# Kernel tuning notes

Hardware: AMD Instinct MI355X
Metric: run time of the kernel (lower is better)

Reference implementation:

```python
import jax, jax.numpy as jnp
import numpy as np

B, T, L, DC, DW, H, V = 128, 256, 4, 128, 128, 256, 6000
NEG = -1e30

def _lstm(x, c, h, kernel, bias):
    # TF BasicLSTMCell, forget_bias=0, gate order i, j, f, o
    z = jnp.concatenate([x, h], axis=-1) @ kernel + bias
    i, j, f, o = jnp.split(z, 4, axis=-1)
    nc = c * jax.nn.sigmoid(f) + jax.nn.sigmoid(i) * jnp.tanh(j)
    nh = jnp.tanh(nc) * jax.nn.sigmoid(o)
    return nc, nh

def _forward(chars, char_emb, reset_W, reset_b, com_W, com_b, lstm_kernel, lstm_bias, pred_W, pred_b, score_U, bos):
    Bn, Tn = chars.shape
    dt = char_emb.dtype
    # init agenda entry: BoS vector through LSTM from zero state
    c0 = jnp.zeros((Bn, H), dt)
    h0 = jnp.zeros((Bn, H), dt)
    x0 = jnp.broadcast_to(bos, (Bn, DW))
    c1, h1 = _lstm(x0, c0, h0, lstm_kernel, lstm_bias)
    pred0 = jnp.tanh(h1 @ pred_W + pred_b)
    # rolling buffer over the last L agenda entries (slot w-1 = position t-w)
    buf_pred = jnp.repeat(pred0[:, None, :], L, axis=1)
    buf_c = jnp.repeat(c1[:, None, :], L, axis=1)
    buf_h = jnp.repeat(h1[:, None, :], L, axis=1)
    # windows[t, b, j] = char at position t-j (age j), front-padded
    padded = jnp.pad(chars, ((0, 0), (L - 1, 0)))
    gi = jnp.arange(Tn)[:, None] + (L - 1) - jnp.arange(L)[None, :]
    windows = jnp.transpose(padded[:, gi], (1, 0, 2))  # [T, B, L]
    wlens = jnp.arange(1, L + 1)
    cmask = (jnp.arange(L)[None, :] < wlens[:, None]).astype(dt)  # [W, C]
    inv_len = (1.0 / wlens).astype(dt)

    def step(carry, xs):
        buf_pred, buf_c, buf_h = carry
        window, t = xs
        emb = char_emb[window]  # [B, L, DC] (ages 0..L-1)
        # per-wlen reset gate (separate weights per word length)
        g = jax.nn.sigmoid(jnp.einsum('bcd,wde->bwce', emb, reset_W) + reset_b[None, :, None, :])
        proj = jnp.tanh(jnp.einsum('bwcd,de->bwce', g * emb[:, None], com_W) + com_b)  # [B,W,C,DW]
        word = jnp.einsum('bwce,wc->bwe', proj, cmask) * inv_len[None, :, None]  # [B,W,DW] mean over the wlen chars
        score = jnp.sum((buf_pred + score_U) * word, axis=-1)  # [B,W] local score vs prev prediction
        score = jnp.where((wlens <= t + 1)[None, :], score, NEG)
        best = jnp.argmax(score, axis=1)  # greedy choice of word length
        b3 = best[:, None, None]
        word_b = jnp.take_along_axis(word, b3, axis=1)[:, 0]
        c_prev = jnp.take_along_axis(buf_c, b3, axis=1)[:, 0]
        h_prev = jnp.take_along_axis(buf_h, b3, axis=1)[:, 0]
        nc, nh = _lstm(word_b, c_prev, h_prev, lstm_kernel, lstm_bias)
        npred = jnp.tanh(nh @ pred_W + pred_b)
        carry = (jnp.concatenate([npred[:, None], buf_pred[:, :-1]], axis=1),
                 jnp.concatenate([nc[:, None], buf_c[:, :-1]], axis=1),
                 jnp.concatenate([nh[:, None], buf_h[:, :-1]], axis=1))
        best_score = jnp.take_along_axis(score, best[:, None], axis=1)[:, 0]
        return carry, (best_score, best + 1)

    _, (scores, wl) = jax.lax.scan(step, (buf_pred, buf_c, buf_h), (windows, jnp.arange(Tn)))
    return scores.T, wl.T  # [B,T] best local score, [B,T] chosen word length

def setup_inputs() -> dict:
    key = jax.random.key(0)
    ks = jax.random.split(key, 12)
    f = lambda k, s: 0.1 * jax.random.normal(k, s, dtype=jnp.float32)
    return {
        'chars': jax.random.randint(ks[0], (B, T), 0, V, dtype=jnp.int32),
        'char_emb': f(ks[1], (V, DC)),
        'reset_W': f(ks[2], (L, DC, DC)),
        'reset_b': f(ks[3], (L, DC)),
        'com_W': f(ks[4], (DC, DW)),
        'com_b': f(ks[5], (DW,)),
        'lstm_kernel': f(ks[6], (DW + H, 4 * H)),
        'lstm_bias': jnp.zeros((4 * H,), jnp.float32),
        'pred_W': f(ks[7], (H, DW)),
        'pred_b': f(ks[8], (DW,)),
        'score_U': f(ks[9], (DW,)),
        'bos': f(ks[10], (DW,)),
    }

def reference(chars, char_emb, reset_W, reset_b, com_W, com_b, lstm_kernel, lstm_bias, pred_W, pred_b, score_U, bos):
    return _forward(chars, char_emb, reset_W, reset_b, com_W, com_b, lstm_kernel, lstm_bias, pred_W, pred_b, score_U, bos)
```

## Files before the change

### kernel.cpp

```cpp
#include <hip/hip_runtime.h>

#define B_ 128
#define T_ 256
#define L_ 4
#define DC_ 128
#define DW_ 128
#define H_ 256
#define V_ 6000
#define Z4_ 1024
#define S_ 4
#define R_ 2
#define G_ 64
#define NEGF -1e30f

#define WS_VTAB  4096
#define WS_NH    (WS_VTAB + V_*L_*DW_*4)
#define WS_PP    (WS_NH + (size_t)2*G_*R_*H_*8)

typedef unsigned long long u64w;

__device__ __forceinline__ float sigm(float x) { return 1.0f / (1.0f + expf(-x)); }
__device__ __forceinline__ void pub64(u64w* p, float v, unsigned stamp) {
  u64w w = ((u64w)__float_as_uint(v) << 32) | (u64w)stamp;
  __hip_atomic_store(p, w, __ATOMIC_RELAXED, __HIP_MEMORY_SCOPE_AGENT);
}
__device__ __forceinline__ u64w ld64(const u64w* p) {
  return __hip_atomic_load(p, __ATOMIC_RELAXED, __HIP_MEMORY_SCOPE_AGENT);
}
__device__ __forceinline__ float hi32(u64w w) {
  return __uint_as_float((unsigned)(w >> 32));
}
__device__ __forceinline__ float bcast(float v, int l) {
  return __int_as_float(__builtin_amdgcn_readlane(__float_as_int(v), l));
}
__device__ __forceinline__ int amax4(const float* sc) {
  float bs = sc[0]; int bw = 0;
  if (sc[1] > bs) { bs = sc[1]; bw = 1; }
  if (sc[2] > bs) { bs = sc[2]; bw = 2; }
  if (sc[3] > bs) { bs = sc[3]; bw = 3; }
  return bw;
}
__device__ __forceinline__ float invlen(int w) {
  return (w == 0) ? 1.0f : (w == 1) ? 0.5f : (w == 2) ? (1.0f / 3.0f) : 0.25f;
}

__global__ __launch_bounds__(512) void vtab_kernel(
    const float* __restrict__ char_emb, const float* __restrict__ reset_W,
    const float* __restrict__ reset_b, const float* __restrict__ com_W,
    const float* __restrict__ com_b, float* __restrict__ Vtab)
{
  const int v = blockIdx.x;
  const int tid = threadIdx.x;
  const int w = tid >> 7;
  const int e = tid & 127;
  __shared__ float emb[DC_];
  __shared__ float ge[L_][DC_];
  if (tid < DC_) emb[tid] = char_emb[v * DC_ + tid];
  __syncthreads();
  float acc = reset_b[w * DC_ + e];
  const float* W = reset_W + (size_t)w * DC_ * DC_;
  #pragma unroll 8
  for (int k = 0; k < DC_; ++k) acc = fmaf(emb[k], W[k * DC_ + e], acc);
  ge[w][e] = sigm(acc) * emb[e];
  __syncthreads();
  float acc2 = com_b[e];
  #pragma unroll 8
  for (int k = 0; k < DC_; ++k) acc2 = fmaf(ge[w][k], com_W[k * DW_ + e], acc2);
  Vtab[((size_t)v * L_ + w) * DW_ + e] = tanhf(acc2);
}

__global__ __launch_bounds__(512, 2) void seq_kernel(
    const int* __restrict__ chars, const float* __restrict__ Vtab,
    const float* __restrict__ Kmat, const float* __restrict__ lstm_bias,
    const float* __restrict__ pred_W, const float* __restrict__ pred_b,
    const float* __restrict__ score_U, const float* __restrict__ bos,
    float* __restrict__ out, u64w* __restrict__ nh_mb, u64w* __restrict__ pp_mb)
{
  const int blk = blockIdx.x;
  const int s = blk >> 6;
  const int g = blk & 63;
  const int tid = threadIdx.x;
  const int lane = tid & 63;
  const int wv = tid >> 6;
  const int c = tid & 255;
  const int koff = (tid < 256) ? 0 : 192;
  const int colg = (c >> 6) * H_ + s * 64 + (c & 63);
  const int row0 = g * R_;

  float wreg[192];
  #pragma unroll
  for (int i = 0; i < 192; ++i)
    wreg[i] = Kmat[(size_t)(koff + i) * Z4_ + colg];

  __shared__ float ringVt[R_][4][512];
  __shared__ float pring[4][R_][DW_];
  __shared__ float zring[4][R_][256];
  __shared__ float cring[4][R_][64];
  __shared__ float zhA[R_][256];
  __shared__ float zhB[R_][256];
  __shared__ float zxL[R_][256];
  __shared__ float predWL[64][128];
  __shared__ float h1tmp[H_];
  __shared__ int   charsL[R_][T_];
  __shared__ float biasC[256], UL[128], pbL[128];
  __shared__ float scL[R_][L_];
  __shared__ float nhLowL[2][64];
  __shared__ float nhUpL[6][64];
  __shared__ int   stampLow, stampUp;

  if (tid == 0) { stampLow = 0; stampUp = 0; }
  if (tid < 256) biasC[tid] = lstm_bias[(tid >> 6) * H_ + s * 64 + (tid & 63)];
  if (tid < 128) { UL[tid] = score_U[tid]; pbL[tid] = pred_b[tid]; }
  for (int i = tid; i < 64 * 128; i += 512)
    predWL[i >> 7][i & 127] = pred_W[(size_t)(s * 64 + (i >> 7)) * DW_ + (i & 127)];
  for (int i = tid; i < R_ * T_; i += 512)
    charsL[i >> 8][i & 255] = chars[(row0 + (i >> 8)) * T_ + (i & 255)];
  for (int i = tid; i < R_ * 4 * 512; i += 512) ((float*)ringVt)[i] = 0.0f;
  __syncthreads();

  {
    float* zb = &zring[0][0][0];
    for (int c2 = tid; c2 < Z4_; c2 += 512) {
      float a = lstm_bias[c2];
      #pragma unroll 8
      for (int k = 0; k < DC_; ++k) a = fmaf(bos[k], Kmat[(size_t)k * Z4_ + c2], a);
      zb[c2] = a;
    }
    __syncthreads();
    if (tid < H_) {
      float zi = zb[tid], zj = zb[H_ + tid], zo = zb[3 * H_ + tid];
      float nc = sigm(zi) * tanhf(zj);
      float nh = tanhf(nc) * sigm(zo);
      h1tmp[tid] = nh;
      int hl = tid - s * 64;
      if (hl >= 0 && hl < 64) {
        #pragma unroll
        for (int q = 0; q < 4; ++q)
          #pragma unroll
          for (int r = 0; r < R_; ++r) cring[q][r][hl] = nc;
      }
    }
    __syncthreads();
    {
      int kq = tid >> 7, e = tid & 127;
      float a = 0.0f;
      #pragma unroll 8
      for (int k = kq * 64; k < kq * 64 + 64; ++k)
        a = fmaf(h1tmp[k], pred_W[(size_t)k * DW_ + e], a);
      ((float*)zhA)[kq * 128 + e] = a;
    }
    __syncthreads();
    if (tid < 128) {
      const float* pa = (const float*)zhA;
      float p = tanhf(pbL[tid] + pa[tid] + pa[128 + tid] + pa[256 + tid] + pa[384 + tid]);
      #pragma unroll
      for (int q = 0; q < 4; ++q)
        #pragma unroll
        for (int r = 0; r < R_; ++r) pring[q][r][tid] = p;
    }
    __syncthreads();
    {
      float a = 0.0f;
      if (tid < 256) {
        #pragma unroll
        for (int k = 0; k < 64; ++k) a = fmaf(h1tmp[k], wreg[128 + k], a);
      } else {
        #pragma unroll
        for (int k = 0; k < 192; ++k) a = fmaf(h1tmp[64 + k], wreg[k], a);
      }
      __syncthreads();
      if (tid < 256) zhA[0][c] = a; else zhB[0][c] = a;
    }
    __syncthreads();
    if (tid < 256) {
      float z1 = zhA[0][tid] + zhB[0][tid];
      #pragma unroll
      for (int q = 0; q < 4; ++q)
        #pragma unroll
        for (int r = 0; r < R_; ++r) zring[q][r][tid] = z1;
    }
    __syncthreads();
  }

  for (int t = 0; t < T_; ++t) {
    const int slot = t & 3;
    const int parR = (t - 1) & 1;
    const int parW = t & 1;
    const unsigned stR = (unsigned)t;
    const unsigned stW = (unsigned)(t + 1);

    if ((wv >> 1) == 1) {
      int i2 = tid & 127;
      #pragma unroll
      for (int r = 0; r < R_; ++r) {
        const float* vp = Vtab + (size_t)charsL[r][t] * 512;
        #pragma unroll
        for (int q = 0; q < 4; ++q) ringVt[r][slot][q * 128 + i2] = vp[q * 128 + i2];
      }
    }

    if (t > 0) {
      const u64w* nb = nh_mb + ((size_t)parR * G_ + g) * (R_ * H_);
      if (wv < 2) {
        u64w nw0, nw1;
        for (;;) {
          nw0 = ld64(nb + lane);
          nw1 = ld64(nb + H_ + lane);
          int ok = ((unsigned)nw0 == stR) & ((unsigned)nw1 == stR);
          if (__all(ok)) break;
          __builtin_amdgcn_s_sleep(1);
        }
        float nv0 = hi32(nw0), nv1 = hi32(nw1);
        if (wv == 0) {
          nhLowL[0][lane] = nv0;
          nhLowL[1][lane] = nv1;
          __hip_atomic_store(&stampLow, (int)t, __ATOMIC_RELEASE,
                             __HIP_MEMORY_SCOPE_WORKGROUP);
        }
        float z0 = 0.0f, z1 = 0.0f;
        #pragma unroll
        for (int k = 0; k < 64; ++k) {
          float w = wreg[128 + k];
          z0 = fmaf(bcast(nv0, k), w, z0);
          z1 = fmaf(bcast(nv1, k), w, z1);
        }
        zhA[0][c] = z0; zhA[1][c] = z1;
        const u64w* ppb = pp_mb + ((size_t)parR * G_ + g) * (S_ * R_ * 128) + wv * 128;
        u64w pw0[S_], pw1[S_];
        for (;;) {
          #pragma unroll
          for (int sp = 0; sp < S_; ++sp) {
            pw0[sp] = ld64(ppb + (size_t)sp * (R_ * 128) + lane);
            pw1[sp] = ld64(ppb + (size_t)sp * (R_ * 128) + lane + 64);
          }
          int ok = 1;
          #pragma unroll
          for (int sp = 0; sp < S_; ++sp)
            ok &= ((unsigned)pw0[sp] == stR) & ((unsigned)pw1[sp] == stR);
          if (__all(ok)) break;
          __builtin_amdgcn_s_sleep(1);
        }
        float a0 = pbL[lane], a1 = pbL[lane + 64];
        #pragma unroll
        for (int sp = 0; sp < S_; ++sp) {
          a0 += hi32(pw0[sp]);
          a1 += hi32(pw1[sp]);
        }
        int ps = (t - 1) & 3;
        pring[ps][wv][lane] = tanhf(a0);
        pring[ps][wv][lane + 64] = tanhf(a1);
      } else if (wv < 4) {
        while (__hip_atomic_load(&stampLow, __ATOMIC_ACQUIRE,
                                 __HIP_MEMORY_SCOPE_WORKGROUP) != (int)t)
          __builtin_amdgcn_s_sleep(1);
        float nv0 = nhLowL[0][lane], nv1 = nhLowL[1][lane];
        float z0 = 0.0f, z1 = 0.0f;
        #pragma unroll
        for (int k = 0; k < 64; ++k) {
          float w = wreg[128 + k];
          z0 = fmaf(bcast(nv0, k), w, z0);
          z1 = fmaf(bcast(nv1, k), w, z1);
        }
        zhA[0][c] = z0; zhA[1][c] = z1;
      } else if (wv == 4) {
        u64w nw[2][3];
        for (;;) {
          #pragma unroll
          for (int r = 0; r < 2; ++r)
            #pragma unroll
            for (int j = 0; j < 3; ++j)
              nw[r][j] = ld64(nb + (size_t)r * H_ + 64 + j * 64 + lane);
          int ok = 1;
          #pragma unroll
          for (int r = 0; r < 2; ++r)
            #pragma unroll
            for (int j = 0; j < 3; ++j)
              ok &= ((unsigned)nw[r][j] == stR);
          if (__all(ok)) break;
          __builtin_amdgcn_s_sleep(1);
        }
        #pragma unroll
        for (int r = 0; r < 2; ++r)
          #pragma unroll
          for (int j = 0; j < 3; ++j)
            nhUpL[r * 3 + j][lane] = hi32(nw[r][j]);
        __hip_atomic_store(&stampUp, (int)t, __ATOMIC_RELEASE,
                           __HIP_MEMORY_SCOPE_WORKGROUP);
        float a0 = 0.0f, a1 = 0.0f;
        #pragma unroll
        for (int j = 0; j < 3; ++j) {
          float nv0 = hi32(nw[0][j]), nv1 = hi32(nw[1][j]);
          #pragma unroll
          for (int k = 0; k < 64; ++k) {
            float w = wreg[j * 64 + k];
            a0 = fmaf(bcast(nv0, k), w, a0);
            a1 = fmaf(bcast(nv1, k), w, a1);
          }
        }
        zhB[0][c] = a0; zhB[1][c] = a1;
      } else {
        while (__hip_atomic_load(&stampUp, __ATOMIC_ACQUIRE,
                                 __HIP_MEMORY_SCOPE_WORKGROUP) != (int)t)
          __builtin_amdgcn_s_sleep(1);
        float a0 = 0.0f, a1 = 0.0f;
        #pragma unroll
        for (int j = 0; j < 3; ++j) {
          float nv0 = nhUpL[j][lane], nv1 = nhUpL[3 + j][lane];
          #pragma unroll
          for (int k = 0; k < 64; ++k) {
            float w = wreg[j * 64 + k];
            a0 = fmaf(bcast(nv0, k), w, a0);
            a1 = fmaf(bcast(nv1, k), w, a1);
          }
        }
        zhB[0][c] = a0; zhB[1][c] = a1;
      }
    }
    __syncthreads();

    if (t > 0) {
      int r = tid >> 8, cc = tid & 255;
      zring[(t - 1) & 3][r][cc] = zhA[r][cc] + zhB[r][cc];
    }
    {
      int r = wv >> 2, w = wv & 3;
      int ps = (t - 1 - w) & 3;
      float il = invlen(w);
      float acc = 0.0f;
      #pragma unroll
      for (int hf = 0; hf < 2; ++hf) {
        int e = lane + hf * 64;
        float sa = 0.0f;
        #pragma unroll
        for (int c2 = 0; c2 < L_; ++c2)
          if (c2 <= w) sa += ringVt[r][(t - c2) & 3][w * 128 + e];
        acc = fmaf(pring[ps][r][e] + UL[e], sa * il, acc);
      }
      #pragma unroll
      for (int off = 32; off; off >>= 1) acc += __shfl_down(acc, off);
      if (lane == 0) scL[r][w] = (w <= t) ? acc : NEGF;
    }
    __syncthreads();

    if (tid < 256) {
      float vt0[2], vt1[2];
      #pragma unroll
      for (int r = 0; r < 2; ++r) {
        int bw = amax4(scL[r]);
        float il = invlen(bw);
        float v0 = 0.f, v1 = 0.f;
        #pragma unroll
        for (int c2 = 0; c2 < L_; ++c2)
          if (c2 <= bw) {
            v0 += ringVt[r][(t - c2) & 3][bw * 128 + lane];
            v1 += ringVt[r][(t - c2) & 3][bw * 128 + 64 + lane];
          }
        vt0[r] = v0 * il; vt1[r] = v1 * il;
      }
      float a0 = 0.f, a1 = 0.f;
      #pragma unroll
      for (int k = 0; k < 64; ++k) {
        float w0 = wreg[k], w1 = wreg[64 + k];
        a0 = fmaf(bcast(vt0[0], k), w0, a0);
        a1 = fmaf(bcast(vt0[1], k), w0, a1);
        a0 = fmaf(bcast(vt1[0], k), w1, a0);
        a1 = fmaf(bcast(vt1[1], k), w1, a1);
      }
      zxL[0][c] = a0; zxL[1][c] = a1;
      if (s == 0 && tid < R_) {
        int bw = amax4(scL[tid]);
        out[(row0 + tid) * T_ + t] = scL[tid][bw];
        out[B_ * T_ + (row0 + tid) * T_ + t] = (float)(bw + 1);
      }
    }
    __syncthreads();

    if (tid < 128) {
      __builtin_amdgcn_s_setprio(1);
      int r = wv, hl = lane;
      int bw = amax4(scL[r]);
      int zs = (t - 1 - bw) & 3;
      float zg[4];
      #pragma unroll
      for (int gi = 0; gi < 4; ++gi) {
        int cc = gi * 64 + hl;
        zg[gi] = biasC[cc] + zring[zs][r][cc] + zxL[r][cc];
      }
      float cp = cring[zs][r][hl];
      float nc = cp * sigm(zg[2]) + sigm(zg[0]) * tanhf(zg[1]);
      float nh = tanhf(nc) * sigm(zg[3]);
      pub64(&nh_mb[((size_t)parW * G_ + g) * (R_ * H_) + (size_t)r * H_ + s * 64 + hl],
            nh, stW);
      cring[slot][r][hl] = nc;
      float p0 = 0.f, p1 = 0.f;
      #pragma unroll
      for (int kk = 0; kk < 64; ++kk) {
        float nb2 = bcast(nh, kk);
        p0 = fmaf(nb2, predWL[kk][lane], p0);
        p1 = fmaf(nb2, predWL[kk][lane + 64], p1);
      }
      u64w* pb = pp_mb + ((size_t)parW * G_ + g) * (S_ * R_ * 128)
               + (size_t)s * (R_ * 128) + (size_t)r * 128;
      pub64(pb + lane, p0, stW);
      pub64(pb + lane + 64, p1, stW);
      __builtin_amdgcn_s_setprio(0);
    }
  }
}

extern "C" void kernel_launch(void* const* d_in, const int* in_sizes, int n_in,
                              void* d_out, int out_size, void* d_ws, size_t ws_size,
                              hipStream_t stream) {
  const int*   chars     = (const int*)d_in[0];
  const float* char_emb  = (const float*)d_in[1];
  const float* reset_W   = (const float*)d_in[2];
  const float* reset_b   = (const float*)d_in[3];
  const float* com_W     = (const float*)d_in[4];
  const float* com_b     = (const float*)d_in[5];
  const float* lstm_k    = (const float*)d_in[6];
  const float* lstm_bias = (const float*)d_in[7];
  const float* pred_W    = (const float*)d_in[8];
  const float* pred_b    = (const float*)d_in[9];
  const float* score_U   = (const float*)d_in[10];
  const float* bos       = (const float*)d_in[11];

  char* ws = (char*)d_ws;
  float* Vtab = (float*)(ws + WS_VTAB);
  u64w* nh_mb = (u64w*)(ws + WS_NH);
  u64w* pp_mb = (u64w*)(ws + WS_PP);

  vtab_kernel<<<V_, 512, 0, stream>>>(char_emb, reset_W, reset_b, com_W, com_b, Vtab);
  seq_kernel<<<256, 512, 0, stream>>>(chars, Vtab, lstm_k, lstm_bias, pred_W,
                                      pred_b, score_U, bos, (float*)d_out,
                                      nh_mb, pp_mb);
}
```

Before: 2.082 ms.

## Fold score computation into producer warps and drop a per-step barrier

The separate phase that computed the word-length scores after a barrier is moved into the first warp-role branch. Warps 0-1 compute the length-1 score from registers, warps 2-3 compute lengths 2-4 next to the ring fill, and the zring update moves into the idle threads of the next phase. This removes one __syncthreads per timestep on the serial recurrence path. The cost is extra global reads of the Vtab rows and more work on some warps. It also depends on the intra-warp ordering of the ringVt writes against the later reads from other slots.

```diff
diff --git a/kernel.cpp b/kernel.cpp
--- a/kernel.cpp
+++ b/kernel.cpp
@@ -189,19 +189,13 @@
     const unsigned stR = (unsigned)t;
     const unsigned stW = (unsigned)(t + 1);
 
-    if ((wv >> 1) == 1) {
-      int i2 = tid & 127;
-      #pragma unroll
-      for (int r = 0; r < R_; ++r) {
-        const float* vp = Vtab + (size_t)charsL[r][t] * 512;
-        #pragma unroll
-        for (int q = 0; q < 4; ++q) ringVt[r][slot][q * 128 + i2] = vp[q * 128 + i2];
-      }
-    }
-
-    if (t > 0) {
-      const u64w* nb = nh_mb + ((size_t)parR * G_ + g) * (R_ * H_);
-      if (wv < 2) {
+    if (wv < 2) {
+      const int r = wv;
+      const float* vp0 = Vtab + (size_t)charsL[r][t] * 512;
+      float vva = vp0[lane];
+      float vvb = vp0[64 + lane];
+      if (t > 0) {
+        const u64w* nb = nh_mb + ((size_t)parR * G_ + g) * (R_ * H_);
         u64w nw0, nw1;
         for (;;) {
           nw0 = ld64(nb + lane);
@@ -249,7 +243,55 @@
         int ps = (t - 1) & 3;
         pring[ps][wv][lane] = tanhf(a0);
         pring[ps][wv][lane + 64] = tanhf(a1);
-      } else if (wv < 4) {
+      }
+      {
+        int ps = (t - 1) & 3;
+        float il = invlen(0);
+        float acc = 0.0f;
+        { float sa = vva;
+          acc = fmaf(pring[ps][r][lane] + UL[lane], sa * il, acc); }
+        { float sa = vvb;
+          acc = fmaf(pring[ps][r][lane + 64] + UL[lane + 64], sa * il, acc); }
+        #pragma unroll
+        for (int off = 32; off; off >>= 1) acc += __shfl_down(acc, off);
+        if (lane == 0) scL[r][0] = acc;
+      }
+    } else if (wv < 4) {
+      const int rsc = wv - 2;
+      int i2 = tid & 127;
+      #pragma unroll
+      for (int r = 0; r < R_; ++r) {
+        const float* vp = Vtab + (size_t)charsL[r][t] * 512;
+        #pragma unroll
+        for (int q = 0; q < 4; ++q) ringVt[r][slot][q * 128 + i2] = vp[q * 128 + i2];
+      }
+      const float* vpr = Vtab + (size_t)charsL[rsc][t] * 512;
+      float va[3], vb[3];
+      #pragma unroll
+      for (int w = 1; w <= 3; ++w) {
+        va[w - 1] = vpr[w * 128 + lane];
+        vb[w - 1] = vpr[w * 128 + 64 + lane];
+      }
+      #pragma unroll
+      for (int w = 1; w <= 3; ++w) {
+        int ps = (t - 1 - w) & 3;
+        float il = invlen(w);
+        float acc = 0.0f;
+        { float sa = va[w - 1];
+          #pragma unroll
+          for (int c2 = 1; c2 < L_; ++c2)
+            if (c2 <= w) sa += ringVt[rsc][(t - c2) & 3][w * 128 + lane];
+          acc = fmaf(pring[ps][rsc][lane] + UL[lane], sa * il, acc); }
+        { float sa = vb[w - 1];
+          #pragma unroll
+          for (int c2 = 1; c2 < L_; ++c2)
+            if (c2 <= w) sa += ringVt[rsc][(t - c2) & 3][w * 128 + 64 + lane];
+          acc = fmaf(pring[ps][rsc][lane + 64] + UL[lane + 64], sa * il, acc); }
+        #pragma unroll
+        for (int off = 32; off; off >>= 1) acc += __shfl_down(acc, off);
+        if (lane == 0) scL[rsc][w] = (w <= t) ? acc : NEGF;
+      }
+      if (t > 0) {
         while (__hip_atomic_load(&stampLow, __ATOMIC_ACQUIRE,
                                  __HIP_MEMORY_SCOPE_WORKGROUP) != (int)t)
           __builtin_amdgcn_s_sleep(1);
@@ -262,7 +304,10 @@
           z1 = fmaf(bcast(nv1, k), w, z1);
         }
         zhA[0][c] = z0; zhA[1][c] = z1;
-      } else if (wv == 4) {
+      }
+    } else if (wv == 4) {
+      if (t > 0) {
+        const u64w* nb = nh_mb + ((size_t)parR * G_ + g) * (R_ * H_);
         u64w nw[2][3];
         for (;;) {
           #pragma unroll
@@ -298,7 +343,9 @@
           }
         }
         zhB[0][c] = a0; zhB[1][c] = a1;
-      } else {
+      }
+    } else {
+      if (t > 0) {
         while (__hip_atomic_load(&stampUp, __ATOMIC_ACQUIRE,
                                  __HIP_MEMORY_SCOPE_WORKGROUP) != (int)t)
           __builtin_amdgcn_s_sleep(1);
@@ -315,30 +362,6 @@
         }
         zhB[0][c] = a0; zhB[1][c] = a1;
       }
-    }
-    __syncthreads();
-
-    if (t > 0) {
-      int r = tid >> 8, cc = tid & 255;
-      zring[(t - 1) & 3][r][cc] = zhA[r][cc] + zhB[r][cc];
-    }
-    {
-      int r = wv >> 2, w = wv & 3;
-      int ps = (t - 1 - w) & 3;
-      float il = invlen(w);
-      float acc = 0.0f;
-      #pragma unroll
-      for (int hf = 0; hf < 2; ++hf) {
-        int e = lane + hf * 64;
-        float sa = 0.0f;
-        #pragma unroll
-        for (int c2 = 0; c2 < L_; ++c2)
-          if (c2 <= w) sa += ringVt[r][(t - c2) & 3][w * 128 + e];
-        acc = fmaf(pring[ps][r][e] + UL[e], sa * il, acc);
-      }
-      #pragma unroll
-      for (int off = 32; off; off >>= 1) acc += __shfl_down(acc, off);
-      if (lane == 0) scL[r][w] = (w <= t) ? acc : NEGF;
     }
     __syncthreads();
 
@@ -372,6 +395,9 @@
         out[(row0 + tid) * T_ + t] = scL[tid][bw];
         out[B_ * T_ + (row0 + tid) * T_ + t] = (float)(bw + 1);
       }
+    } else if (t > 0) {
+      zring[(t - 1) & 3][0][c] = zhA[0][c] + zhB[0][c];
+      zring[(t - 1) & 3][1][c] = zhA[1][c] + zhB[1][c];
     }
     __syncthreads();
 
```

Measured after the change: 1.946 ms. -6.6%, faster.
